# Kernel tuning notes

Hardware: AMD Instinct MI355X
Metric: run time of the kernel (lower is better)

The kernel has to match this reference:

```python
import jax, jax.numpy as jnp
import numpy as np

B, S, D = 4, 2048, 1024
H, HD = 16, 64
WINDOW = 256


def setup_inputs() -> dict:
    key = jax.random.key(0)
    ks = jax.random.split(key, 5)
    scale = 1.0 / np.sqrt(D)
    return {
        "hidden_states": jax.random.normal(ks[0], (B, S, D), dtype=jnp.float32),
        "Wq": jax.random.normal(ks[1], (D, D), dtype=jnp.float32) * scale,
        "Wk": jax.random.normal(ks[2], (D, D), dtype=jnp.float32) * scale,
        "Wv": jax.random.normal(ks[3], (D, D), dtype=jnp.float32) * scale,
        "Wo": jax.random.normal(ks[4], (D, D), dtype=jnp.float32) * scale,
        "bo": jnp.zeros((D,), dtype=jnp.float32),
    }


def reference(hidden_states, Wq, Wk, Wv, Wo, bo):
    # q/k/v projections (no bias), torch Linear: x @ W.T
    q = hidden_states @ Wq.T  # [B,S,D]
    k = hidden_states @ Wk.T
    v = hidden_states @ Wv.T

    def split_heads(t):  # [B,S,D] -> [B,H,S,HD]
        return t.reshape(B, S, H, HD).transpose(0, 2, 1, 3)

    q, k, v = split_heads(q), split_heads(k), split_heads(v)

    # NOTE: original code does NOT scale by 1/sqrt(head_dim)
    scores = jnp.einsum("bhqd,bhkd->bhqk", q.astype(jnp.float32), k.astype(jnp.float32))

    # local causal band mask: keep j <= i and i - j < WINDOW
    i = jnp.arange(S)[:, None]
    j = jnp.arange(S)[None, :]
    band = (j <= i) & (i - j < WINDOW)  # [S,S] bool
    mask_value = jnp.finfo(scores.dtype).min
    scores = jnp.where(band[None, None, :, :], scores, mask_value)

    attn = jax.nn.softmax(scores, axis=-1).astype(v.dtype)
    ctx = jnp.einsum("bhqk,bhkd->bhqd", attn, v)  # [B,H,S,HD]

    # merge heads -> [B,S,D]
    ctx = ctx.transpose(0, 2, 1, 3).reshape(B, S, D)
    out = ctx @ Wo.T + bo
    return out
```

## Files before the change

kernel.cpp:

```cpp
#include <hip/hip_runtime.h>
#include <hip/hip_bf16.h>
#include <cstdint>
#include <cstddef>

#define S_LEN   2048
#define BATCH   4
#define NHEAD   16
#define HDIM    64
#define DMODEL  1024
#define WIN     256
#define PQ      72

typedef __bf16 bf16x8 __attribute__((ext_vector_type(8)));
typedef float f32x4 __attribute__((ext_vector_type(4)));
typedef unsigned short u16x4 __attribute__((ext_vector_type(4)));
typedef unsigned short u16x8 __attribute__((ext_vector_type(8)));

__device__ __forceinline__ unsigned short f2bf(float x) {
  union { float f; unsigned u; } c; c.f = x;
  unsigned r = (c.u + 0x7fffu + ((c.u >> 16) & 1u)) >> 16;
  return (unsigned short)r;
}

__device__ __forceinline__ void gld_lds16(const void* g, void* l) {
  __builtin_amdgcn_global_load_lds(
      (__attribute__((address_space(1))) void*)g,
      (__attribute__((address_space(3))) void*)l, 16, 0, 0);
}

__global__ __launch_bounds__(256) void convert_kernel(
    const float* __restrict__ s0, const float* __restrict__ s1,
    const float* __restrict__ s2, const float* __restrict__ s3,
    const float* __restrict__ s4,
    unsigned short* __restrict__ d0, unsigned short* __restrict__ d1,
    unsigned short* __restrict__ d2, unsigned short* __restrict__ d3,
    unsigned short* __restrict__ d4) {
  const int z = blockIdx.y;
  const float* s; unsigned short* d; long n;
  if      (z == 0) { s = s0; d = d0; n = (long)8192 * 1024; }
  else if (z == 1) { s = s1; d = d1; n = (long)1024 * 1024; }
  else if (z == 2) { s = s2; d = d2; n = (long)1024 * 1024; }
  else if (z == 3) { s = s3; d = d3; n = (long)1024 * 1024; }
  else             { s = s4; d = d4; n = (long)1024 * 1024; }
  const long base = ((long)blockIdx.x * 256 + threadIdx.x) * 16;
  if (base >= n) return;
#pragma unroll
  for (int i = 0; i < 4; ++i) {
    const float4 f = *(const float4*)(s + base + i * 4);
    u16x4 ov;
    ov.x = f2bf(f.x); ov.y = f2bf(f.y); ov.z = f2bf(f.z); ov.w = f2bf(f.w);
    *(u16x4*)(d + base + i * 4) = ov;
  }
}

template <int MODE>
__device__ __forceinline__ void gemm_pipe_core(
    const unsigned short* __restrict__ A, const unsigned short* __restrict__ B,
    void* __restrict__ C, const float* __restrict__ bias,
    int M, int N, int K, unsigned short* __restrict__ ls) {
  const int m0 = blockIdx.x * 128;
  const int n0 = blockIdx.y * 256;
  const int tid  = threadIdx.x;
  const int lane = tid & 63;
  const int wid  = tid >> 6;
  const int quad = lane >> 4, l16 = lane & 15;
  const int wm = wid >> 2, wn = wid & 3;

  const int REG = 24576;

  const int srow   = tid >> 3;
  const int schunk = tid & 7;
  const int scol   = ((schunk ^ ((tid >> 4) & 7)) << 3);

  f32x4 acc[4][4];
#pragma unroll
  for (int i = 0; i < 4; ++i)
#pragma unroll
    for (int j = 0; j < 4; ++j) acc[i][j] = f32x4{0.f, 0.f, 0.f, 0.f};

  const int NT = K >> 6;

#pragma unroll
  for (int tt = 0; tt < 2; ++tt) {
    const int k0 = tt << 6;
#pragma unroll
    for (int q = 0; q < 2; ++q) {
      const int row = srow + 64 * q;
      gld_lds16(A + (size_t)(m0 + row) * K + k0 + scol,
                ls + tt * REG + row * 64 + schunk * 8);
    }
#pragma unroll
    for (int q = 0; q < 4; ++q) {
      const int row = srow + 64 * q;
      gld_lds16(B + (size_t)(n0 + row) * K + k0 + scol,
                ls + tt * REG + 8192 + row * 64 + schunk * 8);
    }
  }
  asm volatile("s_waitcnt vmcnt(6)" ::: "memory");
  __builtin_amdgcn_s_barrier();
  __builtin_amdgcn_sched_barrier(0);

  for (int t = 0; t < NT; ++t) {
    const int rt = t % 3;
    const unsigned short* la = ls + rt * REG;
    const unsigned short* lb = la + 8192;
    const int ts = t + 2;
    const int rs = ts % 3;
    const bool doStage = ts < NT;
    const int k0s = ts << 6;
    unsigned short* da = ls + rs * REG;

    {
      bf16x8 af[4], bfr[4];
#pragma unroll
      for (int mi = 0; mi < 4; ++mi)
        af[mi] = *(const bf16x8*)(la + (wm * 64 + mi * 16 + l16) * 64 +
                                  ((quad ^ (l16 >> 1)) << 3));
#pragma unroll
      for (int ni = 0; ni < 4; ++ni)
        bfr[ni] = *(const bf16x8*)(lb + (wn * 64 + ni * 16 + l16) * 64 +
                                   ((quad ^ (l16 >> 1)) << 3));
      if (doStage) {
#pragma unroll
        for (int q = 0; q < 2; ++q) {
          const int row = srow + 64 * q;
          gld_lds16(A + (size_t)(m0 + row) * K + k0s + scol,
                    da + row * 64 + schunk * 8);
        }
        gld_lds16(B + (size_t)(n0 + srow) * K + k0s + scol,
                  da + 8192 + srow * 64 + schunk * 8);
      }
      __builtin_amdgcn_s_setprio(1);
#pragma unroll
      for (int mi = 0; mi < 4; ++mi)
#pragma unroll
        for (int ni = 0; ni < 4; ++ni)
          acc[mi][ni] = __builtin_amdgcn_mfma_f32_16x16x32_bf16(
              af[mi], bfr[ni], acc[mi][ni], 0, 0, 0);
      __builtin_amdgcn_s_setprio(0);
    }

    {
      bf16x8 af[4], bfr[4];
#pragma unroll
      for (int mi = 0; mi < 4; ++mi)
        af[mi] = *(const bf16x8*)(la + (wm * 64 + mi * 16 + l16) * 64 +
                                  (((4 + quad) ^ (l16 >> 1)) << 3));
#pragma unroll
      for (int ni = 0; ni < 4; ++ni)
        bfr[ni] = *(const bf16x8*)(lb + (wn * 64 + ni * 16 + l16) * 64 +
                                   (((4 + quad) ^ (l16 >> 1)) << 3));
      if (doStage) {
#pragma unroll
        for (int q = 1; q < 4; ++q) {
          const int row = srow + 64 * q;
          gld_lds16(B + (size_t)(n0 + row) * K + k0s + scol,
                    da + 8192 + row * 64 + schunk * 8);
        }
      }
      __builtin_amdgcn_s_setprio(1);
#pragma unroll
      for (int mi = 0; mi < 4; ++mi)
#pragma unroll
        for (int ni = 0; ni < 4; ++ni)
          acc[mi][ni] = __builtin_amdgcn_mfma_f32_16x16x32_bf16(
              af[mi], bfr[ni], acc[mi][ni], 0, 0, 0);
      __builtin_amdgcn_s_setprio(0);
    }
    if (t + 2 < NT) {
      asm volatile("s_waitcnt vmcnt(6)" ::: "memory");
    } else if (t + 1 < NT) {
      asm volatile("s_waitcnt vmcnt(0)" ::: "memory");
    }
    __builtin_amdgcn_s_barrier();
    __builtin_amdgcn_sched_barrier(0);
  }

#pragma unroll
  for (int mi = 0; mi < 4; ++mi) {
    if (MODE == 2) {
      const int mB = m0 + wm * 64 + mi * 16 + quad * 4;
      const int bq = mB >> 11, s = mB & 2047;
#pragma unroll
      for (int ni = 0; ni < 4; ++ni) {
        const int n = n0 + wn * 64 + ni * 16 + l16;
        u16x4 w;
        w[0] = f2bf(acc[mi][ni][0]); w[1] = f2bf(acc[mi][ni][1]);
        w[2] = f2bf(acc[mi][ni][2]); w[3] = f2bf(acc[mi][ni][3]);
        *(u16x4*)((unsigned short*)C +
                  (((size_t)((bq << 4) | (n >> 6)) * 64 + (n & 63)) << 11) + s) = w;
      }
    } else {
#pragma unroll
      for (int r = 0; r < 4; ++r) {
        const int m = m0 + wm * 64 + mi * 16 + quad * 4 + r;
#pragma unroll
        for (int ni = 0; ni < 4; ++ni) {
          const int n = n0 + wn * 64 + ni * 16 + l16;
          const float vv = acc[mi][ni][r];
          if (MODE == 0) {
            ((unsigned short*)C)[(size_t)m * N + n] = f2bf(vv);
          } else {
            ((float*)C)[(size_t)m * N + n] = vv + bias[n];
          }
        }
      }
    }
  }
}

__global__ __launch_bounds__(512, 2) void gemm_qkv_kernel(
    const unsigned short* __restrict__ A,
    const unsigned short* __restrict__ B0, const unsigned short* __restrict__ B1,
    const unsigned short* __restrict__ B2,
    unsigned short* __restrict__ C0, unsigned short* __restrict__ C1,
    unsigned short* __restrict__ Cv, int M, int N, int K) {
  __shared__ unsigned short ls[3 * 24576];
  if (blockIdx.z == 2) {
    gemm_pipe_core<2>(A, B2, Cv, nullptr, M, N, K, ls);
  } else {
    const unsigned short* B = blockIdx.z == 0 ? B0 : B1;
    unsigned short*       C = blockIdx.z == 0 ? C0 : C1;
    gemm_pipe_core<0>(A, B, C, nullptr, M, N, K, ls);
  }
}

template <int MODE>
__device__ __forceinline__ void gemm_bt_core(
    const unsigned short* __restrict__ A, const unsigned short* __restrict__ B,
    void* __restrict__ C, const float* __restrict__ bias,
    int M, int N, int K,
    unsigned short* __restrict__ lsA, unsigned short* __restrict__ lsB) {
  const int m0 = blockIdx.x * 128;
  const int n0 = blockIdx.y * 128;
  const int tid  = threadIdx.x;
  const int wave = tid >> 6, lane = tid & 63;
  const int quad = lane >> 4, l16 = lane & 15;
  const int wm = wave >> 1, wn = wave & 1;

  f32x4 acc[4][4];
#pragma unroll
  for (int i = 0; i < 4; ++i)
#pragma unroll
    for (int j = 0; j < 4; ++j) acc[i][j] = f32x4{0.f, 0.f, 0.f, 0.f};

  const int trow   = tid >> 3;
  const int tchunk = tid & 7;
  const int swz_w  = (trow >> 1) & 7;
  const int scol   = ((tchunk ^ swz_w) << 3);
  const int swz_r  = (l16 >> 1) & 7;

  for (int k0 = 0; k0 < K; k0 += 64) {
    __syncthreads();
#pragma unroll
    for (int c = 0; c < 4; ++c) {
      const int row  = trow + 32 * c;
      const int flat = row * 64 + tchunk * 8;
      gld_lds16(A + (size_t)(m0 + row) * K + k0 + scol, lsA + flat);
      gld_lds16(B + (size_t)(n0 + row) * K + k0 + scol, lsB + flat);
    }
    __syncthreads();

#pragma unroll
    for (int s2 = 0; s2 < 2; ++s2) {
      bf16x8 af[4], bfr[4];
#pragma unroll
      for (int mi = 0; mi < 4; ++mi)
        af[mi] = *(const bf16x8*)(lsA + (wm * 64 + mi * 16 + l16) * 64 +
                                  (((s2 * 4 + quad) ^ swz_r) << 3));
#pragma unroll
      for (int ni = 0; ni < 4; ++ni)
        bfr[ni] = *(const bf16x8*)(lsB + (wn * 64 + ni * 16 + l16) * 64 +
                                   (((s2 * 4 + quad) ^ swz_r) << 3));
#pragma unroll
      for (int mi = 0; mi < 4; ++mi)
#pragma unroll
        for (int ni = 0; ni < 4; ++ni)
          acc[mi][ni] = __builtin_amdgcn_mfma_f32_16x16x32_bf16(
              af[mi], bfr[ni], acc[mi][ni], 0, 0, 0);
    }
  }

#pragma unroll
  for (int mi = 0; mi < 4; ++mi) {
#pragma unroll
    for (int r = 0; r < 4; ++r) {
      const int m = m0 + wm * 64 + mi * 16 + quad * 4 + r;
#pragma unroll
      for (int ni = 0; ni < 4; ++ni) {
        const int n = n0 + wn * 64 + ni * 16 + l16;
        const float vv = acc[mi][ni][r];
        if (MODE == 0) {
          ((unsigned short*)C)[(size_t)m * N + n] = f2bf(vv);
        } else {
          ((float*)C)[(size_t)m * N + n] = vv + bias[n];
        }
      }
    }
  }
}

__global__ __launch_bounds__(256) void gemm_out_kernel(
    const unsigned short* __restrict__ A, const unsigned short* __restrict__ B,
    float* __restrict__ C, const float* __restrict__ bias, int M, int N, int K) {
  __shared__ unsigned short lsA[128 * 64];
  __shared__ unsigned short lsB[128 * 64];
  gemm_bt_core<1>(A, B, C, bias, M, N, K, lsA, lsB);
}

__global__ __launch_bounds__(256) void attn_kernel(
    const unsigned short* __restrict__ q, const unsigned short* __restrict__ k,
    const unsigned short* __restrict__ vt, unsigned short* __restrict__ ctx) {
  const int bh = blockIdx.y;
  const int b = bh >> 4, h = bh & 15;
  const int i0 = blockIdx.x * 128;
  const int tid  = threadIdx.x;
  const int wave = tid >> 6, lane = tid & 63;
  const int quad = lane >> 4, l16 = lane & 15;

  __shared__ unsigned short lsQ[128 * PQ];
  __shared__ unsigned short lsK[64 * PQ];
  __shared__ unsigned short lsVp[64 * PQ];

  {
    const int r = tid >> 1, cb = (tid & 1) * 32;
    const unsigned short* src =
        q + ((size_t)(b * S_LEN + i0 + r) * DMODEL + h * HDIM + cb);
    *(u16x8*)(lsQ + r * PQ + cb)      = *(const u16x8*)src;
    *(u16x8*)(lsQ + r * PQ + cb + 8)  = *(const u16x8*)(src + 8);
    *(u16x8*)(lsQ + r * PQ + cb + 16) = *(const u16x8*)(src + 16);
    *(u16x8*)(lsQ + r * PQ + cb + 24) = *(const u16x8*)(src + 24);
  }

  const int rr = tid >> 2, cb = (tid & 3) * 16;
  const int jhi  = cb >> 4;
  const int vbase = (jhi >> 1) * 32 + (jhi & 1) * 4;

  const int jb0 = (i0 >= WIN) ? ((i0 - WIN + 1) >> 6) : 0;
  const int jb1 = (i0 + 127) >> 6;
  const int jbi = i0 >> 6;

  u16x8 pk0, pk1, pv0, pv1;
  {
    const int j0 = jb0 * 64;
    const unsigned short* ks =
        k + ((size_t)(b * S_LEN + j0 + rr) * DMODEL + h * HDIM + cb);
    pk0 = *(const u16x8*)ks;
    pk1 = *(const u16x8*)(ks + 8);
    const unsigned short* vs =
        vt + ((size_t)(bh * HDIM + rr) * S_LEN + j0 + cb);
    pv0 = *(const u16x8*)vs;
    pv1 = *(const u16x8*)(vs + 8);
  }

  __syncthreads();

  bf16x8 aq[2][2];
#pragma unroll
  for (int t = 0; t < 2; ++t)
#pragma unroll
    for (int s2 = 0; s2 < 2; ++s2)
      aq[t][s2] = *(const bf16x8*)(lsQ + (wave * 32 + t * 16 + l16) * PQ +
                                   s2 * 32 + quad * 8);

  float l_lane[2] = {0.f, 0.f};
  f32x4 o[2][4];
#pragma unroll
  for (int t = 0; t < 2; ++t)
#pragma unroll
    for (int nd = 0; nd < 4; ++nd) o[t][nd] = f32x4{0.f, 0.f, 0.f, 0.f};

  for (int jb = jb0; jb <= jb1; ++jb) {
    const int j0 = jb * 64;
    const bool needMask = !(jb == jbi - 1 || jb == jbi - 2);
    __syncthreads();
    {
      *(u16x8*)(lsK + rr * PQ + cb)     = pk0;
      *(u16x8*)(lsK + rr * PQ + cb + 8) = pk1;
      u16x4 w0, w1, w2, w3;
      w0[0]=pv0[0]; w0[1]=pv0[1]; w0[2]=pv0[2]; w0[3]=pv0[3];
      w1[0]=pv0[4]; w1[1]=pv0[5]; w1[2]=pv0[6]; w1[3]=pv0[7];
      w2[0]=pv1[0]; w2[1]=pv1[1]; w2[2]=pv1[2]; w2[3]=pv1[3];
      w3[0]=pv1[4]; w3[1]=pv1[5]; w3[2]=pv1[6]; w3[3]=pv1[7];
      *(u16x4*)(lsVp + rr * PQ + vbase)      = w0;
      *(u16x4*)(lsVp + rr * PQ + vbase + 8)  = w1;
      *(u16x4*)(lsVp + rr * PQ + vbase + 16) = w2;
      *(u16x4*)(lsVp + rr * PQ + vbase + 24) = w3;
    }
    __syncthreads();

    if (jb < jb1) {
      const int jn = j0 + 64;
      const unsigned short* ks =
          k + ((size_t)(b * S_LEN + jn + rr) * DMODEL + h * HDIM + cb);
      pk0 = *(const u16x8*)ks;
      pk1 = *(const u16x8*)(ks + 8);
      const unsigned short* vs =
          vt + ((size_t)(bh * HDIM + rr) * S_LEN + jn + cb);
      pv0 = *(const u16x8*)vs;
      pv1 = *(const u16x8*)(vs + 8);
    }

    f32x4 st[2][4];
#pragma unroll
    for (int t = 0; t < 2; ++t)
#pragma unroll
      for (int ni = 0; ni < 4; ++ni) st[t][ni] = f32x4{0.f, 0.f, 0.f, 0.f};
    __builtin_amdgcn_s_setprio(1);
#pragma unroll
    for (int s2 = 0; s2 < 2; ++s2) {
      bf16x8 bk[4];
#pragma unroll
      for (int ni = 0; ni < 4; ++ni)
        bk[ni] = *(const bf16x8*)(lsK + (ni * 16 + l16) * PQ + s2 * 32 + quad * 8);
#pragma unroll
      for (int t = 0; t < 2; ++t)
#pragma unroll
        for (int ni = 0; ni < 4; ++ni)
          st[t][ni] = __builtin_amdgcn_mfma_f32_16x16x32_bf16(
              bk[ni], aq[t][s2], st[t][ni], 0, 0, 0);
    }
    __builtin_amdgcn_s_setprio(0);

    bf16x8 ap[2][2];
#pragma unroll
    for (int t = 0; t < 2; ++t) {
      const int iq = i0 + wave * 32 + t * 16 + l16;
      if (needMask) {
#pragma unroll
        for (int ni = 0; ni < 4; ++ni)
#pragma unroll
          for (int r = 0; r < 4; ++r) {
            const int j = j0 + ni * 16 + quad * 4 + r;
            const bool ok = ((unsigned)(iq - j) < (unsigned)WIN);
            const float p = ok ? __expf(fminf(st[t][ni][r], 80.f)) : 0.f;
            st[t][ni][r] = p;
            l_lane[t] += p;
          }
      } else {
#pragma unroll
        for (int ni = 0; ni < 4; ++ni)
#pragma unroll
          for (int r = 0; r < 4; ++r) {
            const float p = __expf(fminf(st[t][ni][r], 80.f));
            st[t][ni][r] = p;
            l_lane[t] += p;
          }
      }
#pragma unroll
      for (int s2 = 0; s2 < 2; ++s2) {
        bf16x8 a;
#pragma unroll
        for (int r = 0; r < 4; ++r) {
          union { unsigned short u; __bf16 h; } c0, c1;
          c0.u = f2bf(st[t][2 * s2][r]);
          c1.u = f2bf(st[t][2 * s2 + 1][r]);
          a[r]     = c0.h;
          a[4 + r] = c1.h;
        }
        ap[t][s2] = a;
      }
    }

    __builtin_amdgcn_s_setprio(1);
#pragma unroll
    for (int s2 = 0; s2 < 2; ++s2) {
      bf16x8 bv[4];
#pragma unroll
      for (int nd = 0; nd < 4; ++nd)
        bv[nd] = *(const bf16x8*)(lsVp + (nd * 16 + l16) * PQ + s2 * 32 + quad * 8);
#pragma unroll
      for (int t = 0; t < 2; ++t)
#pragma unroll
        for (int nd = 0; nd < 4; ++nd)
          o[t][nd] = __builtin_amdgcn_mfma_f32_16x16x32_bf16(
              ap[t][s2], bv[nd], o[t][nd], 0, 0, 0);
    }
    __builtin_amdgcn_s_setprio(0);
  }

#pragma unroll
  for (int t = 0; t < 2; ++t) {
    float l = l_lane[t];
    l += __shfl_xor(l, 16, 64);
    l += __shfl_xor(l, 32, 64);
    const float invl = 1.f / l;
#pragma unroll
    for (int r = 0; r < 4; ++r) {
      const float inv = __shfl(invl, quad * 4 + r, 64);
      const int i = i0 + wave * 32 + t * 16 + quad * 4 + r;
#pragma unroll
      for (int nd = 0; nd < 4; ++nd)
        ctx[(size_t)(b * S_LEN + i) * DMODEL + h * HDIM + nd * 16 + l16] =
            f2bf(o[t][nd][r] * inv);
    }
  }
}

extern "C" void kernel_launch(void* const* d_in, const int* in_sizes, int n_in,
                              void* d_out, int out_size, void* d_ws, size_t ws_size,
                              hipStream_t stream) {
  const float* hs = (const float*)d_in[0];
  const float* Wq = (const float*)d_in[1];
  const float* Wk = (const float*)d_in[2];
  const float* Wv = (const float*)d_in[3];
  const float* Wo = (const float*)d_in[4];
  const float* bo = (const float*)d_in[5];
  float* out = (float*)d_out;

  const size_t MD = (size_t)8192 * 1024;
  const size_t DD = (size_t)1024 * 1024;
  unsigned short* hsb  = (unsigned short*)d_ws;
  unsigned short* wqb  = hsb + MD;
  unsigned short* wkb  = wqb + DD;
  unsigned short* wvb  = wkb + DD;
  unsigned short* wob  = wvb + DD;
  unsigned short* qb   = wob + DD;
  unsigned short* kb   = qb + MD;
  unsigned short* vtb  = kb + MD;
  unsigned short* ctxb = vtb + MD;

  convert_kernel<<<dim3(2048, 5), 256, 0, stream>>>(hs, Wq, Wk, Wv, Wo,
                                                    hsb, wqb, wkb, wvb, wob);
  gemm_qkv_kernel<<<dim3(64, 4, 3), 512, 0, stream>>>(hsb, wqb, wkb, wvb,
                                                      qb, kb, vtb, 8192, 1024, 1024);
  attn_kernel<<<dim3(16, 64), 256, 0, stream>>>(qb, kb, vtb, ctxb);
  gemm_out_kernel<<<dim3(64, 8), 256, 0, stream>>>(ctxb, wob, out, bo,
                                                   8192, 1024, 1024);
}
```

Measured before the change: 218.6 us.

## Reuse pipelined GEMM core for output projection, grid-stride convert, packed bf16 cvt

The output projection now runs on the pipelined 128x256-tile GEMM core already used for QKV (MODE 1 with bias and fp32 store), with 512 threads per block, replacing the simpler single-buffered 128x128 GEMM. The conversion kernel becomes a grid-stride loop over fewer blocks, which cuts the number of blocks that exit early for the small weight matrices. In attention, the bf16 packing of probabilities uses the hardware v_cvt_pk_bf16_f32 instruction in place of manual rounding. This relies on gemm_pipe_core handling MODE 1 correctly, and the grid drops to 256 blocks, which may leave some compute units underused.

```diff
diff --git a/kernel.cpp b/kernel.cpp
--- a/kernel.cpp
+++ b/kernel.cpp
@@ -20,6 +20,12 @@
   union { float f; unsigned u; } c; c.f = x;
   unsigned r = (c.u + 0x7fffu + ((c.u >> 16) & 1u)) >> 16;
   return (unsigned short)r;
+}
+
+__device__ __forceinline__ unsigned cvt_pk_bf16(float lo, float hi) {
+  unsigned r;
+  asm("v_cvt_pk_bf16_f32 %0, %1, %2" : "=v"(r) : "v"(lo), "v"(hi));
+  return r;
 }
 
 __device__ __forceinline__ void gld_lds16(const void* g, void* l) {
@@ -42,14 +48,16 @@
   else if (z == 2) { s = s2; d = d2; n = (long)1024 * 1024; }
   else if (z == 3) { s = s3; d = d3; n = (long)1024 * 1024; }
   else             { s = s4; d = d4; n = (long)1024 * 1024; }
-  const long base = ((long)blockIdx.x * 256 + threadIdx.x) * 16;
-  if (base >= n) return;
-#pragma unroll
-  for (int i = 0; i < 4; ++i) {
-    const float4 f = *(const float4*)(s + base + i * 4);
-    u16x4 ov;
-    ov.x = f2bf(f.x); ov.y = f2bf(f.y); ov.z = f2bf(f.z); ov.w = f2bf(f.w);
-    *(u16x4*)(d + base + i * 4) = ov;
+  const long stride = (long)512 * 256 * 16;
+  for (long base = ((long)blockIdx.x * 256 + threadIdx.x) * 16; base < n;
+       base += stride) {
+#pragma unroll
+    for (int i = 0; i < 4; ++i) {
+      const float4 f = *(const float4*)(s + base + i * 4);
+      u16x4 ov;
+      ov.x = f2bf(f.x); ov.y = f2bf(f.y); ov.z = f2bf(f.z); ov.w = f2bf(f.w);
+      *(u16x4*)(d + base + i * 4) = ov;
+    }
   }
 }
 
@@ -225,87 +233,11 @@
   }
 }
 
-template <int MODE>
-__device__ __forceinline__ void gemm_bt_core(
-    const unsigned short* __restrict__ A, const unsigned short* __restrict__ B,
-    void* __restrict__ C, const float* __restrict__ bias,
-    int M, int N, int K,
-    unsigned short* __restrict__ lsA, unsigned short* __restrict__ lsB) {
-  const int m0 = blockIdx.x * 128;
-  const int n0 = blockIdx.y * 128;
-  const int tid  = threadIdx.x;
-  const int wave = tid >> 6, lane = tid & 63;
-  const int quad = lane >> 4, l16 = lane & 15;
-  const int wm = wave >> 1, wn = wave & 1;
-
-  f32x4 acc[4][4];
-#pragma unroll
-  for (int i = 0; i < 4; ++i)
-#pragma unroll
-    for (int j = 0; j < 4; ++j) acc[i][j] = f32x4{0.f, 0.f, 0.f, 0.f};
-
-  const int trow   = tid >> 3;
-  const int tchunk = tid & 7;
-  const int swz_w  = (trow >> 1) & 7;
-  const int scol   = ((tchunk ^ swz_w) << 3);
-  const int swz_r  = (l16 >> 1) & 7;
-
-  for (int k0 = 0; k0 < K; k0 += 64) {
-    __syncthreads();
-#pragma unroll
-    for (int c = 0; c < 4; ++c) {
-      const int row  = trow + 32 * c;
-      const int flat = row * 64 + tchunk * 8;
-      gld_lds16(A + (size_t)(m0 + row) * K + k0 + scol, lsA + flat);
-      gld_lds16(B + (size_t)(n0 + row) * K + k0 + scol, lsB + flat);
-    }
-    __syncthreads();
-
-#pragma unroll
-    for (int s2 = 0; s2 < 2; ++s2) {
-      bf16x8 af[4], bfr[4];
-#pragma unroll
-      for (int mi = 0; mi < 4; ++mi)
-        af[mi] = *(const bf16x8*)(lsA + (wm * 64 + mi * 16 + l16) * 64 +
-                                  (((s2 * 4 + quad) ^ swz_r) << 3));
-#pragma unroll
-      for (int ni = 0; ni < 4; ++ni)
-        bfr[ni] = *(const bf16x8*)(lsB + (wn * 64 + ni * 16 + l16) * 64 +
-                                   (((s2 * 4 + quad) ^ swz_r) << 3));
-#pragma unroll
-      for (int mi = 0; mi < 4; ++mi)
-#pragma unroll
-        for (int ni = 0; ni < 4; ++ni)
-          acc[mi][ni] = __builtin_amdgcn_mfma_f32_16x16x32_bf16(
-              af[mi], bfr[ni], acc[mi][ni], 0, 0, 0);
-    }
-  }
-
-#pragma unroll
-  for (int mi = 0; mi < 4; ++mi) {
-#pragma unroll
-    for (int r = 0; r < 4; ++r) {
-      const int m = m0 + wm * 64 + mi * 16 + quad * 4 + r;
-#pragma unroll
-      for (int ni = 0; ni < 4; ++ni) {
-        const int n = n0 + wn * 64 + ni * 16 + l16;
-        const float vv = acc[mi][ni][r];
-        if (MODE == 0) {
-          ((unsigned short*)C)[(size_t)m * N + n] = f2bf(vv);
-        } else {
-          ((float*)C)[(size_t)m * N + n] = vv + bias[n];
-        }
-      }
-    }
-  }
-}
-
-__global__ __launch_bounds__(256) void gemm_out_kernel(
+__global__ __launch_bounds__(512, 2) void gemm_out_kernel(
     const unsigned short* __restrict__ A, const unsigned short* __restrict__ B,
     float* __restrict__ C, const float* __restrict__ bias, int M, int N, int K) {
-  __shared__ unsigned short lsA[128 * 64];
-  __shared__ unsigned short lsB[128 * 64];
-  gemm_bt_core<1>(A, B, C, bias, M, N, K, lsA, lsB);
+  __shared__ unsigned short ls[3 * 24576];
+  gemm_pipe_core<1>(A, B, C, bias, M, N, K, ls);
 }
 
 __global__ __launch_bounds__(256) void attn_kernel(
@@ -449,16 +381,12 @@
       }
 #pragma unroll
       for (int s2 = 0; s2 < 2; ++s2) {
-        bf16x8 a;
-#pragma unroll
-        for (int r = 0; r < 4; ++r) {
-          union { unsigned short u; __bf16 h; } c0, c1;
-          c0.u = f2bf(st[t][2 * s2][r]);
-          c1.u = f2bf(st[t][2 * s2 + 1][r]);
-          a[r]     = c0.h;
-          a[4 + r] = c1.h;
-        }
-        ap[t][s2] = a;
+        union { bf16x8 v; unsigned u[4]; } a;
+        a.u[0] = cvt_pk_bf16(st[t][2 * s2][0],     st[t][2 * s2][1]);
+        a.u[1] = cvt_pk_bf16(st[t][2 * s2][2],     st[t][2 * s2][3]);
+        a.u[2] = cvt_pk_bf16(st[t][2 * s2 + 1][0], st[t][2 * s2 + 1][1]);
+        a.u[3] = cvt_pk_bf16(st[t][2 * s2 + 1][2], st[t][2 * s2 + 1][3]);
+        ap[t][s2] = a.v;
       }
     }
 
@@ -520,11 +448,11 @@
   unsigned short* vtb  = kb + MD;
   unsigned short* ctxb = vtb + MD;
 
-  convert_kernel<<<dim3(2048, 5), 256, 0, stream>>>(hs, Wq, Wk, Wv, Wo,
-                                                    hsb, wqb, wkb, wvb, wob);
+  convert_kernel<<<dim3(512, 5), 256, 0, stream>>>(hs, Wq, Wk, Wv, Wo,
+                                                   hsb, wqb, wkb, wvb, wob);
   gemm_qkv_kernel<<<dim3(64, 4, 3), 512, 0, stream>>>(hsb, wqb, wkb, wvb,
                                                       qb, kb, vtb, 8192, 1024, 1024);
   attn_kernel<<<dim3(16, 64), 256, 0, stream>>>(qb, kb, vtb, ctxb);
-  gemm_out_kernel<<<dim3(64, 8), 256, 0, stream>>>(ctxb, wob, out, bo,
+  gemm_out_kernel<<<dim3(64, 4), 512, 0, stream>>>(ctxb, wob, out, bo,
                                                    8192, 1024, 1024);
 }
```

After: 196.9 us. -9.9%, faster.
